# Performance work log

Measured on AMD Instinct MI355X. Metric: run time of the kernel, lower is better.

Reference implementation:

```python
import jax, jax.numpy as jnp
import numpy as np

B, D_IMG, D_NUM, P = 16384, 2048, 256, 128

def setup_inputs() -> dict:
    key = jax.random.key(0)
    ks = jax.random.split(key, 12)
    s = lambda d: 1.0 / np.sqrt(d)
    return {
        "img_feat": jax.random.normal(ks[0], (B, D_IMG), jnp.float32),
        "num_feat": jax.random.normal(ks[1], (B, D_NUM), jnp.float32),
        "Wi1": jax.random.uniform(ks[2], (D_IMG, P), jnp.float32, -s(D_IMG), s(D_IMG)),
        "bi1": jax.random.uniform(ks[3], (P,), jnp.float32, -s(D_IMG), s(D_IMG)),
        "Wi2": jax.random.uniform(ks[4], (P, P), jnp.float32, -s(P), s(P)),
        "bi2": jax.random.uniform(ks[5], (P,), jnp.float32, -s(P), s(P)),
        "Wn1": jax.random.uniform(ks[6], (D_NUM, P), jnp.float32, -s(D_NUM), s(D_NUM)),
        "bn1": jax.random.uniform(ks[7], (P,), jnp.float32, -s(D_NUM), s(D_NUM)),
        "Wn2": jax.random.uniform(ks[8], (P, P), jnp.float32, -s(P), s(P)),
        "bn2": jax.random.uniform(ks[9], (P,), jnp.float32, -s(P), s(P)),
        "log_temp": jnp.asarray(np.log(0.1), jnp.float32),
    }

def _mlp(x, W1, b1, W2, b2):
    h = jax.nn.relu(x @ W1 + b1)
    return h @ W2 + b2

def _l2norm(x, eps=1e-12):
    # matches F.normalize(dim=1): x / max(||x||, eps)
    n = jnp.sqrt(jnp.sum(x * x, axis=1, keepdims=True))
    return x / jnp.maximum(n, eps)

def reference(img_feat, num_feat, Wi1, bi1, Wi2, bi2, Wn1, bn1, Wn2, bn2, log_temp):
    temp = jnp.exp(log_temp)
    ip = _l2norm(_mlp(img_feat, Wi1, bi1, Wi2, bi2))  # [B, P]
    npj = _l2norm(_mlp(num_feat, Wn1, bn1, Wn2, bn2))  # [B, P]
    logits = (ip @ npj.T) / temp                        # [B, B]
    # symmetric cross-entropy with labels = arange(B): targets on the diagonal
    lse_rows = jax.nn.logsumexp(logits, axis=1)  # i2n
    lse_cols = jax.nn.logsumexp(logits, axis=0)  # n2i (logits.T rows)
    diag = jnp.diagonal(logits)
    loss_i2n = jnp.mean(lse_rows - diag)
    loss_n2i = jnp.mean(lse_cols - diag)
    return (loss_i2n + loss_n2i) * 0.5
```

## Files before the change

kernel.cpp:

```cpp
#include <hip/hip_runtime.h>
#include <hip/hip_bf16.h>

typedef __bf16 bf16_t;
typedef __bf16 bf16x8 __attribute__((ext_vector_type(8)));
typedef __bf16 bf16x4 __attribute__((ext_vector_type(4)));
typedef float f32x4 __attribute__((ext_vector_type(4)));

#define NB 16384
#define PP 128
#define NSPLIT 16
#define CG (NB / NSPLIT)
#define NT (CG / 128)

__device__ inline bf16x8 ld8(const bf16_t* p) { return *(const bf16x8*)p; }

__device__ inline void gload_lds16(const bf16_t* g, bf16_t* l) {
  __builtin_amdgcn_global_load_lds(
      (const __attribute__((address_space(1))) unsigned int*)g,
      (__attribute__((address_space(3))) unsigned int*)l, 16, 0, 0);
}

__global__ void transpose_all(const float* __restrict__ Wi1, const float* __restrict__ Wn1,
                              const float* __restrict__ Wi2, const float* __restrict__ Wn2,
                              bf16_t* __restrict__ Wi1t, bf16_t* __restrict__ Wn1t,
                              bf16_t* __restrict__ Wi2t, bf16_t* __restrict__ Wn2t) {
  int idx = blockIdx.x * 256 + threadIdx.x;
  if (idx < 2048 * 128) { int k = idx >> 7, n = idx & 127; Wi1t[n * 2048 + k] = (bf16_t)Wi1[idx]; return; }
  idx -= 2048 * 128;
  if (idx < 256 * 128)  { int k = idx >> 7, n = idx & 127; Wn1t[n * 256 + k]  = (bf16_t)Wn1[idx]; return; }
  idx -= 256 * 128;
  if (idx < 128 * 128)  { int k = idx >> 7, n = idx & 127; Wi2t[n * 128 + k]  = (bf16_t)Wi2[idx]; return; }
  idx -= 128 * 128;
  if (idx < 128 * 128)  { int k = idx >> 7, n = idx & 127; Wn2t[n * 128 + k]  = (bf16_t)Wn2[idx]; }
}

__global__ __launch_bounds__(256, 2) void mlp1_kernel(
    const float* __restrict__ X, const bf16_t* __restrict__ Wt,
    const float* __restrict__ bias, bf16_t* __restrict__ H, int K) {
  __shared__ bf16_t As[32 * 64];
  __shared__ bf16_t Bs[128 * 64];
  const int t = threadIdx.x, l = t & 63, wid = t >> 6;
  const int wm = wid >> 1, wn = wid & 1;
  const int row0 = blockIdx.x * 32;

  f32x4 acc[4];
#pragma unroll
  for (int j = 0; j < 4; j++) acc[j] = (f32x4){0.f, 0.f, 0.f, 0.f};

  for (int k0 = 0; k0 < K; k0 += 64) {
    __syncthreads();
#pragma unroll
    for (int i = 0; i < 2; i++) {
      int s = t + i * 256;
      int r = s >> 4, c4 = s & 15;
      const float4 f = *(const float4*)(X + (size_t)(row0 + r) * K + k0 + c4 * 4);
      bf16x4 pk;
      pk[0] = (bf16_t)f.x; pk[1] = (bf16_t)f.y; pk[2] = (bf16_t)f.z; pk[3] = (bf16_t)f.w;
      int chunk = c4 >> 1, half = c4 & 1;
      *(bf16x4*)(As + r * 64 + (chunk ^ (r & 7)) * 8 + half * 4) = pk;
    }
#pragma unroll
    for (int i = 0; i < 4; i++) {
      int s = t + i * 256;
      int r = s >> 3, c = s & 7;
      bf16x8 v = ld8(Wt + (size_t)r * K + k0 + c * 8);
      *(bf16x8*)(Bs + r * 64 + (c ^ (r & 7)) * 8) = v;
    }
    __syncthreads();
#pragma unroll
    for (int ks = 0; ks < 2; ks++) {
      int r = wm * 16 + (l & 15);
      int c = ks * 4 + (l >> 4);
      bf16x8 a = ld8(As + r * 64 + (c ^ (r & 7)) * 8);
#pragma unroll
      for (int nt = 0; nt < 4; nt++) {
        int rb = wn * 64 + nt * 16 + (l & 15);
        bf16x8 b = ld8(Bs + rb * 64 + (c ^ (rb & 7)) * 8);
        acc[nt] = __builtin_amdgcn_mfma_f32_16x16x32_bf16(a, b, acc[nt], 0, 0, 0);
      }
    }
  }
  int rbase = row0 + wm * 16 + ((l >> 4) << 2);
#pragma unroll
  for (int nt = 0; nt < 4; nt++) {
    int col = wn * 64 + nt * 16 + (l & 15);
    float bv = bias[col];
#pragma unroll
    for (int r4 = 0; r4 < 4; r4++) {
      float v = acc[nt][r4] + bv;
      H[(size_t)(rbase + r4) * PP + col] = (bf16_t)fmaxf(v, 0.f);
    }
  }
}

__global__ __launch_bounds__(256, 2) void mlp2_norm_kernel(
    const bf16_t* __restrict__ Hin, const bf16_t* __restrict__ W2t,
    const float* __restrict__ bias, bf16_t* __restrict__ Out) {
  __shared__ bf16_t As[32 * 128];
  __shared__ bf16_t Bs[128 * 128];
  __shared__ float rnorm[32];
  const int t = threadIdx.x, l = t & 63, wid = t >> 6;
  const int wm = wid >> 1, wn = wid & 1;
  const int row0 = blockIdx.x * 32;
  if (t < 32) rnorm[t] = 0.f;
#pragma unroll
  for (int i = 0; i < 2; i++) {
    int s = t + i * 256;
    int r = s >> 4, c = s & 15;
    bf16x8 v = ld8(Hin + (size_t)(row0 + r) * 128 + c * 8);
    *(bf16x8*)(As + r * 128 + (c ^ (r & 7)) * 8) = v;
  }
#pragma unroll
  for (int i = 0; i < 8; i++) {
    int s = t + i * 256;
    int r = s >> 4, c = s & 15;
    bf16x8 v = ld8(W2t + (size_t)r * 128 + c * 8);
    *(bf16x8*)(Bs + r * 128 + (c ^ (r & 7)) * 8) = v;
  }
  __syncthreads();
  f32x4 acc[4];
#pragma unroll
  for (int j = 0; j < 4; j++) acc[j] = (f32x4){0.f, 0.f, 0.f, 0.f};
#pragma unroll
  for (int ks = 0; ks < 4; ks++) {
    int r = wm * 16 + (l & 15);
    int c = ks * 4 + (l >> 4);
    bf16x8 a = ld8(As + r * 128 + (c ^ (r & 7)) * 8);
#pragma unroll
    for (int nt = 0; nt < 4; nt++) {
      int rb = wn * 64 + nt * 16 + (l & 15);
      bf16x8 b = ld8(Bs + rb * 128 + (c ^ (rb & 7)) * 8);
      acc[nt] = __builtin_amdgcn_mfma_f32_16x16x32_bf16(a, b, acc[nt], 0, 0, 0);
    }
  }
  float vv[4][4];
#pragma unroll
  for (int nt = 0; nt < 4; nt++) {
    int col = wn * 64 + nt * 16 + (l & 15);
    float bv = bias[col];
#pragma unroll
    for (int r4 = 0; r4 < 4; r4++) vv[nt][r4] = acc[nt][r4] + bv;
  }
#pragma unroll
  for (int r4 = 0; r4 < 4; r4++) {
    float p = 0.f;
#pragma unroll
    for (int nt = 0; nt < 4; nt++) p += vv[nt][r4] * vv[nt][r4];
    p += __shfl_xor(p, 1); p += __shfl_xor(p, 2);
    p += __shfl_xor(p, 4); p += __shfl_xor(p, 8);
    if ((l & 15) == 0) atomicAdd(&rnorm[wm * 16 + ((l >> 4) << 2) + r4], p);
  }
  __syncthreads();
#pragma unroll
  for (int r4 = 0; r4 < 4; r4++) {
    int rl = wm * 16 + ((l >> 4) << 2) + r4;
    float sc = 1.f / fmaxf(sqrtf(rnorm[rl]), 1e-12f);
#pragma unroll
    for (int nt = 0; nt < 4; nt++) {
      int col = wn * 64 + nt * 16 + (l & 15);
      int swcol = (((col >> 3) ^ (rl & 7)) << 3) | (col & 7);
      Out[(size_t)(row0 + rl) * 128 + swcol] = (bf16_t)(vv[nt][r4] * sc);
    }
  }
}

__global__ __launch_bounds__(256, 2) void logits_split(
    const bf16_t* __restrict__ IP, const bf16_t* __restrict__ NP,
    const float* __restrict__ log_temp, float* __restrict__ rowpart,
    float* __restrict__ colpart, float* __restrict__ diag) {
  __shared__ bf16_t As[128 * 128];
  __shared__ bf16_t Bs[128 * 128];
  __shared__ float colred[2][CG];
  __shared__ float rowred[2][128];
  int bid = blockIdx.x;
  int sw = (bid & 7) * (128 * NSPLIT / 8) + (bid >> 3);
  int bm = sw >> 4, g = sw & (NSPLIT - 1);
  const int t = threadIdx.x, l = t & 63, wid = t >> 6;
  const int wm = wid >> 1, wn = wid & 1;
  const float invt = __expf(-log_temp[0]);

#pragma unroll
  for (int i = 0; i < 8; i++) {
    int s = t + i * 256;
    gload_lds16(IP + (size_t)bm * (128 * 128) + s * 8, As + s * 8);
  }
#pragma unroll
  for (int i = 0; i < 8; i++) {
    int s = t + i * 256;
    gload_lds16(NP + (size_t)(g * NT) * (128 * 128) + s * 8, Bs + s * 8);
  }
  __syncthreads();

  float racc[4][4];
#pragma unroll
  for (int a = 0; a < 4; a++)
#pragma unroll
    for (int b = 0; b < 4; b++) racc[a][b] = 0.f;

#pragma unroll 1
  for (int tl = 0; tl < NT; tl++) {
    f32x4 acc[4][4];
#pragma unroll
    for (int i = 0; i < 4; i++)
#pragma unroll
      for (int j = 0; j < 4; j++) acc[i][j] = (f32x4){0.f, 0.f, 0.f, 0.f};
#pragma unroll
    for (int ks = 0; ks < 4; ks++) {
      int c = ks * 4 + (l >> 4);
      bf16x8 a[4];
#pragma unroll
      for (int mt = 0; mt < 4; mt++) {
        int r = wm * 64 + mt * 16 + (l & 15);
        a[mt] = ld8(As + r * 128 + (c ^ (r & 7)) * 8);
      }
#pragma unroll
      for (int nt = 0; nt < 4; nt++) {
        int rb = wn * 64 + nt * 16 + (l & 15);
        bf16x8 b = ld8(Bs + rb * 128 + (c ^ (rb & 7)) * 8);
#pragma unroll
        for (int mt = 0; mt < 4; mt++)
          acc[mt][nt] = __builtin_amdgcn_mfma_f32_16x16x32_bf16(a[mt], b, acc[mt][nt], 0, 0, 0);
      }
    }
    __syncthreads();
    if (tl + 1 < NT) {
#pragma unroll
      for (int i = 0; i < 8; i++) {
        int s = t + i * 256;
        gload_lds16(NP + (size_t)(g * NT + tl + 1) * (128 * 128) + s * 8, Bs + s * 8);
      }
    }
    int bn_t = g * NT + tl;
    if (bn_t == bm && wm == wn) {
#pragma unroll
      for (int mt = 0; mt < 4; mt++)
#pragma unroll
        for (int nt = 0; nt < 4; nt++)
#pragma unroll
          for (int r4 = 0; r4 < 4; r4++) {
            int gr = bm * 128 + wm * 64 + mt * 16 + ((l >> 4) << 2) + r4;
            int gc = bn_t * 128 + wn * 64 + nt * 16 + (l & 15);
            if (gr == gc) diag[gr] = acc[mt][nt][r4] * invt;
          }
    }
#pragma unroll
    for (int mt = 0; mt < 4; mt++)
#pragma unroll
      for (int nt = 0; nt < 4; nt++)
#pragma unroll
        for (int r4 = 0; r4 < 4; r4++)
          acc[mt][nt][r4] = __expf(fmaf(acc[mt][nt][r4], invt, -invt));
#pragma unroll
    for (int mt = 0; mt < 4; mt++)
#pragma unroll
      for (int r4 = 0; r4 < 4; r4++)
        racc[mt][r4] += acc[mt][0][r4] + acc[mt][1][r4] + acc[mt][2][r4] + acc[mt][3][r4];
#pragma unroll
    for (int nt = 0; nt < 4; nt++) {
      float cs = 0.f;
#pragma unroll
      for (int mt = 0; mt < 4; mt++)
#pragma unroll
        for (int r4 = 0; r4 < 4; r4++) cs += acc[mt][nt][r4];
      cs += __shfl_xor(cs, 16); cs += __shfl_xor(cs, 32);
      if (l < 16) colred[wm][tl * 128 + wn * 64 + nt * 16 + l] = cs;
    }
    __syncthreads();
  }
#pragma unroll
  for (int mt = 0; mt < 4; mt++)
#pragma unroll
    for (int r4 = 0; r4 < 4; r4++) {
      float rs = racc[mt][r4];
      rs += __shfl_xor(rs, 1); rs += __shfl_xor(rs, 2);
      rs += __shfl_xor(rs, 4); rs += __shfl_xor(rs, 8);
      if ((l & 15) == 0)
        rowred[wn][wm * 64 + mt * 16 + ((l >> 4) << 2) + r4] = rs;
    }
  __syncthreads();
  if (t < 128)
    rowpart[(size_t)g * NB + bm * 128 + t] = rowred[0][t] + rowred[1][t];
  for (int c = t; c < CG; c += 256)
    colpart[(size_t)bm * NB + g * CG + c] = colred[0][c] + colred[1][c];
}

__global__ void finalize1(const float* __restrict__ rowpart, const float* __restrict__ colpart,
                          const float* __restrict__ diag, float* __restrict__ lossacc) {
  int i = blockIdx.x * 64 + threadIdx.x;
  float rsum = 0.f, csum = 0.f;
#pragma unroll
  for (int g = 0; g < NSPLIT; g++) rsum += rowpart[(size_t)g * NB + i];
#pragma unroll 8
  for (int b = 0; b < 128; b++) csum += colpart[(size_t)b * NB + i];
  float v = 0.5f * (logf(rsum) + logf(csum)) - diag[i];
  for (int m = 1; m < 64; m <<= 1) v += __shfl_xor(v, m);
  if (threadIdx.x == 0) atomicAdd(lossacc, v);
}

__global__ void finalize2(const float* __restrict__ lossacc,
                          const float* __restrict__ log_temp, float* __restrict__ out) {
  out[0] = lossacc[0] / (float)NB + __expf(-log_temp[0]);
}

extern "C" void kernel_launch(void* const* d_in, const int* in_sizes, int n_in,
                              void* d_out, int out_size, void* d_ws, size_t ws_size,
                              hipStream_t stream) {
  const float* img = (const float*)d_in[0];
  const float* num = (const float*)d_in[1];
  const float* Wi1 = (const float*)d_in[2];
  const float* bi1 = (const float*)d_in[3];
  const float* Wi2 = (const float*)d_in[4];
  const float* bi2 = (const float*)d_in[5];
  const float* Wn1 = (const float*)d_in[6];
  const float* bn1 = (const float*)d_in[7];
  const float* Wn2 = (const float*)d_in[8];
  const float* bn2 = (const float*)d_in[9];
  const float* log_temp = (const float*)d_in[10];
  float* out = (float*)d_out;

  char* w = (char*)d_ws;
  bf16_t* ipb   = (bf16_t*)(w);
  bf16_t* npb   = (bf16_t*)(w + (4u << 20));
  bf16_t* h_img = (bf16_t*)(w + (8u << 20));
  bf16_t* h_num = (bf16_t*)(w + (12u << 20));
  float*  colpart = (float*)(w + (8u << 20));
  bf16_t* Wi1t  = (bf16_t*)(w + (16u << 20));
  bf16_t* Wn1t  = (bf16_t*)(w + (16u << 20) + (512u << 10));
  bf16_t* Wi2t  = (bf16_t*)(w + (16u << 20) + (576u << 10));
  bf16_t* Wn2t  = (bf16_t*)(w + (16u << 20) + (640u << 10));
  float*  rowpart = (float*)(w + (16u << 20));
  float*  diag  = (float*)(w + (17u << 20));
  float*  lossacc = (float*)(w + (17u << 20) + (64u << 10));

  hipMemsetAsync(lossacc, 0, sizeof(float), stream);

  transpose_all<<<dim3(1280), 256, 0, stream>>>(Wi1, Wn1, Wi2, Wn2, Wi1t, Wn1t, Wi2t, Wn2t);

  mlp1_kernel<<<dim3(NB / 32), 256, 0, stream>>>(img, Wi1t, bi1, h_img, 2048);
  mlp1_kernel<<<dim3(NB / 32), 256, 0, stream>>>(num, Wn1t, bn1, h_num, 256);
  mlp2_norm_kernel<<<dim3(NB / 32), 256, 0, stream>>>(h_img, Wi2t, bi2, ipb);
  mlp2_norm_kernel<<<dim3(NB / 32), 256, 0, stream>>>(h_num, Wn2t, bn2, npb);

  logits_split<<<dim3(128 * NSPLIT), 256, 0, stream>>>(ipb, npb, log_temp, rowpart, colpart, diag);
  finalize1<<<dim3(NB / 64), 64, 0, stream>>>(rowpart, colpart, diag, lossacc);
  finalize2<<<dim3(1), 1, 0, stream>>>(lossacc, log_temp, out);
}
```

Baseline: 396.4 us.

## Merge MLP launches, double-buffer logits B tiles, keep A fragments in registers

The image and numeric MLP layers now run as single combined launches, and mlp1 uses a K-step of 128. In the logits kernel, the A fragments are held in registers, B tiles shrink to 64 columns and are double-buffered so the next tile loads during compute, and exp is computed as exp2 with a prescaled factor. These changes aim to cut launch overhead and to hide global-to-LDS latency in the dominant logits kernel. The cost is higher register pressure from the A fragments held in registers, and the occupancy hints change as a result.

```diff
diff --git a/kernel.cpp b/kernel.cpp
--- a/kernel.cpp
+++ b/kernel.cpp
@@ -10,7 +10,8 @@
 #define PP 128
 #define NSPLIT 16
 #define CG (NB / NSPLIT)
-#define NT (CG / 128)
+#define BNT 64
+#define NT (CG / BNT)
 
 __device__ inline bf16x8 ld8(const bf16_t* p) { return *(const bf16x8*)p; }
 
@@ -34,48 +35,57 @@
   if (idx < 128 * 128)  { int k = idx >> 7, n = idx & 127; Wn2t[n * 128 + k]  = (bf16_t)Wn2[idx]; }
 }
 
-__global__ __launch_bounds__(256, 2) void mlp1_kernel(
-    const float* __restrict__ X, const bf16_t* __restrict__ Wt,
-    const float* __restrict__ bias, bf16_t* __restrict__ H, int K) {
-  __shared__ bf16_t As[32 * 64];
-  __shared__ bf16_t Bs[128 * 64];
+__global__ __launch_bounds__(256, 4) void mlp1_combined(
+    const float* __restrict__ Ximg, const float* __restrict__ Xnum,
+    const bf16_t* __restrict__ Wit, const bf16_t* __restrict__ Wnt,
+    const float* __restrict__ bi, const float* __restrict__ bn,
+    bf16_t* __restrict__ Himg, bf16_t* __restrict__ Hnum) {
+  __shared__ bf16_t As[32 * 128];
+  __shared__ bf16_t Bs[128 * 128];
+  const int bid = blockIdx.x;
+  const bool isnum = bid >= 512;
+  const float* X = isnum ? Xnum : Ximg;
+  const bf16_t* Wt = isnum ? Wnt : Wit;
+  const float* bias = isnum ? bn : bi;
+  bf16_t* H = isnum ? Hnum : Himg;
+  const int K = isnum ? 256 : 2048;
   const int t = threadIdx.x, l = t & 63, wid = t >> 6;
   const int wm = wid >> 1, wn = wid & 1;
-  const int row0 = blockIdx.x * 32;
+  const int row0 = (bid & 511) * 32;
 
   f32x4 acc[4];
 #pragma unroll
   for (int j = 0; j < 4; j++) acc[j] = (f32x4){0.f, 0.f, 0.f, 0.f};
 
-  for (int k0 = 0; k0 < K; k0 += 64) {
+  for (int k0 = 0; k0 < K; k0 += 128) {
     __syncthreads();
 #pragma unroll
-    for (int i = 0; i < 2; i++) {
+    for (int i = 0; i < 4; i++) {
       int s = t + i * 256;
-      int r = s >> 4, c4 = s & 15;
+      int r = s >> 5, c4 = s & 31;
       const float4 f = *(const float4*)(X + (size_t)(row0 + r) * K + k0 + c4 * 4);
       bf16x4 pk;
       pk[0] = (bf16_t)f.x; pk[1] = (bf16_t)f.y; pk[2] = (bf16_t)f.z; pk[3] = (bf16_t)f.w;
       int chunk = c4 >> 1, half = c4 & 1;
-      *(bf16x4*)(As + r * 64 + (chunk ^ (r & 7)) * 8 + half * 4) = pk;
-    }
-#pragma unroll
-    for (int i = 0; i < 4; i++) {
+      *(bf16x4*)(As + r * 128 + ((chunk ^ (r & 7)) << 3) + half * 4) = pk;
+    }
+#pragma unroll
+    for (int i = 0; i < 8; i++) {
       int s = t + i * 256;
-      int r = s >> 3, c = s & 7;
+      int r = s >> 4, c = s & 15;
       bf16x8 v = ld8(Wt + (size_t)r * K + k0 + c * 8);
-      *(bf16x8*)(Bs + r * 64 + (c ^ (r & 7)) * 8) = v;
+      *(bf16x8*)(Bs + r * 128 + ((c ^ (r & 7)) << 3)) = v;
     }
     __syncthreads();
 #pragma unroll
-    for (int ks = 0; ks < 2; ks++) {
+    for (int ks = 0; ks < 4; ks++) {
       int r = wm * 16 + (l & 15);
       int c = ks * 4 + (l >> 4);
-      bf16x8 a = ld8(As + r * 64 + (c ^ (r & 7)) * 8);
+      bf16x8 a = ld8(As + r * 128 + ((c ^ (r & 7)) << 3));
 #pragma unroll
       for (int nt = 0; nt < 4; nt++) {
         int rb = wn * 64 + nt * 16 + (l & 15);
-        bf16x8 b = ld8(Bs + rb * 64 + (c ^ (rb & 7)) * 8);
+        bf16x8 b = ld8(Bs + rb * 128 + ((c ^ (rb & 7)) << 3));
         acc[nt] = __builtin_amdgcn_mfma_f32_16x16x32_bf16(a, b, acc[nt], 0, 0, 0);
       }
     }
@@ -93,29 +103,37 @@
   }
 }
 
-__global__ __launch_bounds__(256, 2) void mlp2_norm_kernel(
-    const bf16_t* __restrict__ Hin, const bf16_t* __restrict__ W2t,
-    const float* __restrict__ bias, bf16_t* __restrict__ Out) {
+__global__ __launch_bounds__(256, 3) void mlp2_combined(
+    const bf16_t* __restrict__ Himg, const bf16_t* __restrict__ Hnum,
+    const bf16_t* __restrict__ Wi2t, const bf16_t* __restrict__ Wn2t,
+    const float* __restrict__ bi2, const float* __restrict__ bn2,
+    bf16_t* __restrict__ OutI, bf16_t* __restrict__ OutN) {
   __shared__ bf16_t As[32 * 128];
   __shared__ bf16_t Bs[128 * 128];
   __shared__ float rnorm[32];
+  const int bid = blockIdx.x;
+  const bool isnum = bid >= 512;
+  const bf16_t* Hin = isnum ? Hnum : Himg;
+  const bf16_t* W2t = isnum ? Wn2t : Wi2t;
+  const float* bias = isnum ? bn2 : bi2;
+  bf16_t* Out = isnum ? OutN : OutI;
   const int t = threadIdx.x, l = t & 63, wid = t >> 6;
   const int wm = wid >> 1, wn = wid & 1;
-  const int row0 = blockIdx.x * 32;
+  const int row0 = (bid & 511) * 32;
   if (t < 32) rnorm[t] = 0.f;
 #pragma unroll
   for (int i = 0; i < 2; i++) {
     int s = t + i * 256;
     int r = s >> 4, c = s & 15;
     bf16x8 v = ld8(Hin + (size_t)(row0 + r) * 128 + c * 8);
-    *(bf16x8*)(As + r * 128 + (c ^ (r & 7)) * 8) = v;
+    *(bf16x8*)(As + r * 128 + ((c ^ (r & 7)) << 3)) = v;
   }
 #pragma unroll
   for (int i = 0; i < 8; i++) {
     int s = t + i * 256;
     int r = s >> 4, c = s & 15;
     bf16x8 v = ld8(W2t + (size_t)r * 128 + c * 8);
-    *(bf16x8*)(Bs + r * 128 + (c ^ (r & 7)) * 8) = v;
+    *(bf16x8*)(Bs + r * 128 + ((c ^ (r & 7)) << 3)) = v;
   }
   __syncthreads();
   f32x4 acc[4];
@@ -125,11 +143,11 @@
   for (int ks = 0; ks < 4; ks++) {
     int r = wm * 16 + (l & 15);
     int c = ks * 4 + (l >> 4);
-    bf16x8 a = ld8(As + r * 128 + (c ^ (r & 7)) * 8);
+    bf16x8 a = ld8(As + r * 128 + ((c ^ (r & 7)) << 3));
 #pragma unroll
     for (int nt = 0; nt < 4; nt++) {
       int rb = wn * 64 + nt * 16 + (l & 15);
-      bf16x8 b = ld8(Bs + rb * 128 + (c ^ (rb & 7)) * 8);
+      bf16x8 b = ld8(Bs + rb * 128 + ((c ^ (rb & 7)) << 3));
       acc[nt] = __builtin_amdgcn_mfma_f32_16x16x32_bf16(a, b, acc[nt], 0, 0, 0);
     }
   }
@@ -164,12 +182,11 @@
   }
 }
 
-__global__ __launch_bounds__(256, 2) void logits_split(
+__global__ __launch_bounds__(256, 3) void logits_split(
     const bf16_t* __restrict__ IP, const bf16_t* __restrict__ NP,
     const float* __restrict__ log_temp, float* __restrict__ rowpart,
     float* __restrict__ colpart, float* __restrict__ diag) {
-  __shared__ bf16_t As[128 * 128];
-  __shared__ bf16_t Bs[128 * 128];
+  __shared__ bf16_t BsAll[2 * BNT * 128];
   __shared__ float colred[2][CG];
   __shared__ float rowred[2][128];
   int bid = blockIdx.x;
@@ -178,92 +195,97 @@
   const int t = threadIdx.x, l = t & 63, wid = t >> 6;
   const int wm = wid >> 1, wn = wid & 1;
   const float invt = __expf(-log_temp[0]);
+  const float kk = invt * 1.44269504088896f;
 
 #pragma unroll
   for (int i = 0; i < 8; i++) {
     int s = t + i * 256;
-    gload_lds16(IP + (size_t)bm * (128 * 128) + s * 8, As + s * 8);
-  }
-#pragma unroll
-  for (int i = 0; i < 8; i++) {
+    gload_lds16(IP + (size_t)bm * (128 * 128) + s * 8, BsAll + s * 8);
+  }
+  __syncthreads();
+  bf16x8 af[4][4];
+#pragma unroll
+  for (int mt = 0; mt < 4; mt++) {
+    int r = wm * 64 + mt * 16 + (l & 15);
+#pragma unroll
+    for (int ks = 0; ks < 4; ks++) {
+      int c = ks * 4 + (l >> 4);
+      af[mt][ks] = ld8(BsAll + r * 128 + ((c ^ (r & 7)) << 3));
+    }
+  }
+  __syncthreads();
+#pragma unroll
+  for (int i = 0; i < 4; i++) {
     int s = t + i * 256;
-    gload_lds16(NP + (size_t)(g * NT) * (128 * 128) + s * 8, Bs + s * 8);
-  }
-  __syncthreads();
-
-  float racc[4][4];
-#pragma unroll
-  for (int a = 0; a < 4; a++)
-#pragma unroll
-    for (int b = 0; b < 4; b++) racc[a][b] = 0.f;
+    gload_lds16(NP + (size_t)(g * CG) * 128 + s * 8, BsAll + s * 8);
+  }
+  __syncthreads();
+
+  f32x4 racc[4];
+#pragma unroll
+  for (int a = 0; a < 4; a++) racc[a] = (f32x4){0.f, 0.f, 0.f, 0.f};
 
 #pragma unroll 1
   for (int tl = 0; tl < NT; tl++) {
-    f32x4 acc[4][4];
+    bf16_t* Bsc = BsAll + (tl & 1) * (BNT * 128);
+    if (tl + 1 < NT) {
+      bf16_t* Bsn = BsAll + ((tl + 1) & 1) * (BNT * 128);
+      const bf16_t* src = NP + (size_t)(g * CG + (tl + 1) * BNT) * 128;
+#pragma unroll
+      for (int i = 0; i < 4; i++) {
+        int s = t + i * 256;
+        gload_lds16(src + s * 8, Bsn + s * 8);
+      }
+    }
+    f32x4 acc[4][2];
 #pragma unroll
     for (int i = 0; i < 4; i++)
 #pragma unroll
-      for (int j = 0; j < 4; j++) acc[i][j] = (f32x4){0.f, 0.f, 0.f, 0.f};
+      for (int j = 0; j < 2; j++) acc[i][j] = (f32x4){0.f, 0.f, 0.f, 0.f};
 #pragma unroll
     for (int ks = 0; ks < 4; ks++) {
       int c = ks * 4 + (l >> 4);
-      bf16x8 a[4];
+      bf16x8 b[2];
+#pragma unroll
+      for (int nt = 0; nt < 2; nt++) {
+        int rb = wn * 32 + nt * 16 + (l & 15);
+        b[nt] = ld8(Bsc + rb * 128 + ((c ^ (rb & 7)) << 3));
+      }
 #pragma unroll
       for (int mt = 0; mt < 4; mt++) {
-        int r = wm * 64 + mt * 16 + (l & 15);
-        a[mt] = ld8(As + r * 128 + (c ^ (r & 7)) * 8);
-      }
-#pragma unroll
-      for (int nt = 0; nt < 4; nt++) {
-        int rb = wn * 64 + nt * 16 + (l & 15);
-        bf16x8 b = ld8(Bs + rb * 128 + (c ^ (rb & 7)) * 8);
-#pragma unroll
-        for (int mt = 0; mt < 4; mt++)
-          acc[mt][nt] = __builtin_amdgcn_mfma_f32_16x16x32_bf16(a[mt], b, acc[mt][nt], 0, 0, 0);
-      }
-    }
-    __syncthreads();
-    if (tl + 1 < NT) {
-#pragma unroll
-      for (int i = 0; i < 8; i++) {
-        int s = t + i * 256;
-        gload_lds16(NP + (size_t)(g * NT + tl + 1) * (128 * 128) + s * 8, Bs + s * 8);
-      }
-    }
-    int bn_t = g * NT + tl;
-    if (bn_t == bm && wm == wn) {
+        acc[mt][0] = __builtin_amdgcn_mfma_f32_16x16x32_bf16(af[mt][ks], b[0], acc[mt][0], 0, 0, 0);
+        acc[mt][1] = __builtin_amdgcn_mfma_f32_16x16x32_bf16(af[mt][ks], b[1], acc[mt][1], 0, 0, 0);
+      }
+    }
+    const int colbase = g * CG + tl * BNT;
+    if ((colbase >> 7) == bm) {
 #pragma unroll
       for (int mt = 0; mt < 4; mt++)
 #pragma unroll
-        for (int nt = 0; nt < 4; nt++)
+        for (int nt = 0; nt < 2; nt++)
 #pragma unroll
           for (int r4 = 0; r4 < 4; r4++) {
             int gr = bm * 128 + wm * 64 + mt * 16 + ((l >> 4) << 2) + r4;
-            int gc = bn_t * 128 + wn * 64 + nt * 16 + (l & 15);
+            int gc = colbase + wn * 32 + nt * 16 + (l & 15);
             if (gr == gc) diag[gr] = acc[mt][nt][r4] * invt;
           }
     }
 #pragma unroll
     for (int mt = 0; mt < 4; mt++)
 #pragma unroll
-      for (int nt = 0; nt < 4; nt++)
-#pragma unroll
-        for (int r4 = 0; r4 < 4; r4++)
-          acc[mt][nt][r4] = __expf(fmaf(acc[mt][nt][r4], invt, -invt));
-#pragma unroll
-    for (int mt = 0; mt < 4; mt++)
-#pragma unroll
-      for (int r4 = 0; r4 < 4; r4++)
-        racc[mt][r4] += acc[mt][0][r4] + acc[mt][1][r4] + acc[mt][2][r4] + acc[mt][3][r4];
-#pragma unroll
-    for (int nt = 0; nt < 4; nt++) {
-      float cs = 0.f;
-#pragma unroll
-      for (int mt = 0; mt < 4; mt++)
-#pragma unroll
-        for (int r4 = 0; r4 < 4; r4++) cs += acc[mt][nt][r4];
+      for (int nt = 0; nt < 2; nt++) {
+        f32x4 y = acc[mt][nt] * kk - kk;
+#pragma unroll
+        for (int r4 = 0; r4 < 4; r4++) acc[mt][nt][r4] = __builtin_amdgcn_exp2f(y[r4]);
+      }
+#pragma unroll
+    for (int mt = 0; mt < 4; mt++) racc[mt] += acc[mt][0] + acc[mt][1];
+#pragma unroll
+    for (int nt = 0; nt < 2; nt++) {
+      f32x4 cv = (acc[0][nt] + acc[1][nt]) + (acc[2][nt] + acc[3][nt]);
+      float cs = (cv[0] + cv[1]) + (cv[2] + cv[3]);
       cs += __shfl_xor(cs, 16); cs += __shfl_xor(cs, 32);
-      if (l < 16) colred[wm][tl * 128 + wn * 64 + nt * 16 + l] = cs;
+      if (l < 16) colred[wm][tl * BNT + wn * 32 + nt * 16 + l] = cs;
     }
     __syncthreads();
   }
@@ -290,7 +312,7 @@
   float rsum = 0.f, csum = 0.f;
 #pragma unroll
   for (int g = 0; g < NSPLIT; g++) rsum += rowpart[(size_t)g * NB + i];
-#pragma unroll 8
+#pragma unroll 16
   for (int b = 0; b < 128; b++) csum += colpart[(size_t)b * NB + i];
   float v = 0.5f * (logf(rsum) + logf(csum)) - diag[i];
   for (int m = 1; m < 64; m <<= 1) v += __shfl_xor(v, m);
@@ -336,10 +358,8 @@
 
   transpose_all<<<dim3(1280), 256, 0, stream>>>(Wi1, Wn1, Wi2, Wn2, Wi1t, Wn1t, Wi2t, Wn2t);
 
-  mlp1_kernel<<<dim3(NB / 32), 256, 0, stream>>>(img, Wi1t, bi1, h_img, 2048);
-  mlp1_kernel<<<dim3(NB / 32), 256, 0, stream>>>(num, Wn1t, bn1, h_num, 256);
-  mlp2_norm_kernel<<<dim3(NB / 32), 256, 0, stream>>>(h_img, Wi2t, bi2, ipb);
-  mlp2_norm_kernel<<<dim3(NB / 32), 256, 0, stream>>>(h_num, Wn2t, bn2, npb);
+  mlp1_combined<<<dim3(1024), 256, 0, stream>>>(img, num, Wi1t, Wn1t, bi1, bn1, h_img, h_num);
+  mlp2_combined<<<dim3(1024), 256, 0, stream>>>(h_img, h_num, Wi2t, Wn2t, bi2, bn2, ipb, npb);
 
   logits_split<<<dim3(128 * NSPLIT), 256, 0, stream>>>(ipb, npb, log_temp, rowpart, colpart, diag);
   finalize1<<<dim3(NB / 64), 64, 0, stream>>>(rowpart, colpart, diag, lossacc);
```

Measured after the change: 335.1 us. -15.5%, faster.
